# Optimization experiments

Measured on AMD Instinct MI355X. Metric: run time of the kernel, lower is better.

Reference implementation:

```python
import jax, jax.numpy as jnp
import numpy as np

N = 100000
E = 1600000


def _gcn_conv(x, src, dst, norm, W, b, n_nodes):
    # PyG GCNConv: h = x @ W; aggregate normalized messages; add bias.
    h = x @ W                                   # [N, C_out]
    msg = h[src] * norm[:, None]                # [E', C_out] gathered messages
    out = jax.ops.segment_sum(msg, dst, num_segments=n_nodes)
    return out + b


def _norm_coeffs(src, dst, n_nodes):
    # symmetric normalization with self-loops: D^{-1/2} (A+I) D^{-1/2}
    ones = jnp.ones(src.shape[0], dtype=jnp.float32)
    deg = jax.ops.segment_sum(ones, dst, num_segments=n_nodes)
    dis = jnp.where(deg > 0, jax.lax.rsqrt(jnp.maximum(deg, 1.0)), 0.0)
    return dis[src] * dis[dst]


def setup_inputs() -> dict:
    key = jax.random.key(0)
    k1, k2, k3, k4 = jax.random.split(key, 4)
    x = jax.random.normal(k1, (N, 128), dtype=jnp.float32)
    edge_index = jax.random.randint(k2, (2, E), 0, N, dtype=jnp.int64)
    W1 = jax.random.normal(k3, (128, 128), dtype=jnp.float32) * (1.0 / np.sqrt(128))
    b1 = jnp.zeros((128,), dtype=jnp.float32)
    W2 = jax.random.normal(k4, (128, 64), dtype=jnp.float32) * (1.0 / np.sqrt(128))
    b2 = jnp.zeros((64,), dtype=jnp.float32)
    return {"x": x, "edge_index": edge_index, "W1": W1, "b1": b1, "W2": W2, "b2": b2}


def reference(x, edge_index, W1, b1, W2, b2):
    n_nodes = x.shape[0]
    loop = jnp.arange(n_nodes, dtype=edge_index.dtype)
    src = jnp.concatenate([edge_index[0], loop])   # add self-loops
    dst = jnp.concatenate([edge_index[1], loop])
    norm = _norm_coeffs(src, dst, n_nodes)
    h = _gcn_conv(x, src, dst, norm, W1, b1, n_nodes)
    h = jax.nn.relu(h)
    # dropout(p=0.2) is identity in eval mode
    out = _gcn_conv(h, src, dst, norm, W2, b2, n_nodes)
    return out
```

## Files before the change

kernel.cpp:

```cpp
#include <hip/hip_runtime.h>
#include <hip/hip_bf16.h>


typedef short short8v __attribute__((ext_vector_type(8)));
typedef float f32x4   __attribute__((ext_vector_type(4)));

#define BSHIFT 9
#define BSIZE  512
#define CAPSH  14
#define CAP    (1 << CAPSH)

__device__ __forceinline__ short f2bf(float f) {
    unsigned u = __float_as_uint(f);
    return (short)((u + 0x7fffu + ((u >> 16) & 1u)) >> 16);
}
__device__ __forceinline__ unsigned pack2bf(float a, float b) {
    return (unsigned)(unsigned short)f2bf(a) | ((unsigned)(unsigned short)f2bf(b) << 16);
}
__device__ __forceinline__ float bflo(unsigned u) { return __uint_as_float(u << 16); }
__device__ __forceinline__ float bfhi(unsigned u) { return __uint_as_float(u & 0xffff0000u); }

__global__ void k_prep(const float* __restrict__ W1, const float* __restrict__ W2,
                       short* __restrict__ w1t, short* __restrict__ w2t,
                       int* __restrict__ bcur, int nbuck) {
    int b = blockIdx.x;
    int t = threadIdx.x;
    if (b == gridDim.x - 1) {
        if (t < nbuck) bcur[t] = t << CAPSH;
        return;
    }
    int i = b * 256 + t;
    if (i < 128 * 128) {
        int n = i >> 7, k = i & 127;
        w1t[i] = f2bf(W1[k * 128 + n]);
    } else {
        int j = i - 128 * 128;
        int n = j >> 7, k = j & 127;
        w2t[j] = f2bf(W2[k * 64 + n]);
    }
}

__global__ __launch_bounds__(256) void k_bucket(const int* __restrict__ src,
                                                const int* __restrict__ dst,
                                                int* __restrict__ bcur,
                                                unsigned* __restrict__ ebuf,
                                                int E, int nbuck) {
    __shared__ int sdst[4096];
    __shared__ int ssrc[4096];
    __shared__ int hist[256];
    __shared__ int base[256];
    int t = threadIdx.x;
    int e0 = blockIdx.x * 4096;
    for (int i = t; i < nbuck; i += 256) hist[i] = 0;
    for (int i = 0; i < 16; ++i) {
        int k = i * 256 + t;
        int e = e0 + k;
        sdst[k] = (e < E) ? dst[e] : -1;
        ssrc[k] = (e < E) ? src[e] : 0;
    }
    __syncthreads();
    for (int i = 0; i < 16; ++i) {
        int d = sdst[i * 256 + t];
        if (d >= 0) atomicAdd(&hist[d >> BSHIFT], 1);
    }
    __syncthreads();
    for (int b = t; b < nbuck; b += 256) {
        int c = hist[b];
        base[b] = c ? atomicAdd(&bcur[b], c) : 0;
        hist[b] = 0;
    }
    __syncthreads();
    for (int i = 0; i < 16; ++i) {
        int k = i * 256 + t;
        int d = sdst[k];
        if (d >= 0) {
            int bk = d >> BSHIFT;
            int off = atomicAdd(&hist[bk], 1);
            ebuf[base[bk] + off] = ((unsigned)ssrc[k] << BSHIFT) | (unsigned)(d & (BSIZE - 1));
        }
    }
}

__global__ __launch_bounds__(BSIZE) void k_bcsr(const unsigned* __restrict__ ebuf,
                                                const int* __restrict__ bcur,
                                                int* __restrict__ deg,
                                                int* __restrict__ row_ptr,
                                                float* __restrict__ dinv,
                                                unsigned* __restrict__ csr4, int n) {
    __shared__ unsigned edges[CAP];
    __shared__ int hist[BSIZE];
    __shared__ int s[BSIZE];
    __shared__ int cur[BSIZE];
    int b = blockIdx.x;
    int t = threadIdx.x;
    hist[t] = 0;
    __syncthreads();
    int base = b << CAPSH;
    int cnt  = bcur[b] - base;
    int lo = b << BSHIFT;
    for (int k = t; k < cnt; k += BSIZE) {
        unsigned e = ebuf[base + k];
        edges[k] = e;
        atomicAdd(&hist[e & (BSIZE - 1)], 1);
    }
    __syncthreads();
    int v = hist[t];
    s[t] = v;
    __syncthreads();
    for (int off = 1; off < BSIZE; off <<= 1) {
        int add = (t >= off) ? s[t - off] : 0;
        __syncthreads();
        s[t] += add;
        __syncthreads();
    }
    int rp = base + s[t] - v;
    cur[t] = rp;
    int node = lo + t;
    if (node < n) {
        deg[node]     = v;
        row_ptr[node] = rp;
        dinv[node]    = rsqrtf((float)(v + 1));
    }
    __syncthreads();
    for (int k = t; k < cnt; k += BSIZE) {
        unsigned e = edges[k];
        int pos = atomicAdd(&cur[e & (BSIZE - 1)], 1);
        csr4[pos] = e >> BSHIFT;
    }
}

#define LDP 136
__global__ __launch_bounds__(256) void k_gemm1(const float* __restrict__ x,
                                               const short* __restrict__ w1t,
                                               const float* __restrict__ dinv,
                                               short* __restrict__ h, int nrows) {
    __shared__ short xs[64 * LDP];
    __shared__ short wt[128 * LDP];
    int t = threadIdx.x;
    int row0 = blockIdx.x * 64;
    for (int i = 0; i < 16; ++i) {
        int idx = t + i * 256;
        int r = idx >> 5, c4 = idx & 31;
        float4 v = make_float4(0.f, 0.f, 0.f, 0.f);
        if (row0 + r < nrows) v = ((const float4*)x)[(size_t)(row0 + r) * 32 + c4];
        short4 o = make_short4(f2bf(v.x), f2bf(v.y), f2bf(v.z), f2bf(v.w));
        *(short4*)&xs[r * LDP + c4 * 4] = o;
    }
    for (int i = 0; i < 16; ++i) {
        int idx = t + i * 256;
        int n = idx >> 5, c4 = idx & 31;
        *(short4*)&wt[n * LDP + c4 * 4] = ((const short4*)w1t)[idx];
    }
    __syncthreads();
    int wave = t >> 6, lane = t & 63;
    int quad = lane >> 4, c = lane & 15;
    int m0 = wave * 16;
    f32x4 acc[8] = {};
    #pragma unroll
    for (int kc = 0; kc < 4; ++kc) {
        short8v a = *(const short8v*)&xs[(m0 + c) * LDP + kc * 32 + quad * 8];
        #pragma unroll
        for (int nt = 0; nt < 8; ++nt) {
            short8v b = *(const short8v*)&wt[(nt * 16 + c) * LDP + kc * 32 + quad * 8];
            acc[nt] = __builtin_amdgcn_mfma_f32_16x16x32_bf16(a, b, acc[nt], 0, 0, 0);
        }
    }
    #pragma unroll
    for (int r = 0; r < 4; ++r) {
        int row = row0 + m0 + quad * 4 + r;
        if (row < nrows) {
            float dr = dinv[row];
            #pragma unroll
            for (int nt = 0; nt < 8; ++nt)
                h[(size_t)row * 128 + nt * 16 + c] = f2bf(acc[nt][r] * dr);
        }
    }
}

__global__ __launch_bounds__(256) void k_gemm2(const unsigned* __restrict__ aggb,
                                               const float* __restrict__ b1,
                                               const short* __restrict__ w2t,
                                               const float* __restrict__ dinv,
                                               short* __restrict__ h2, int nrows) {
    __shared__ short xs[64 * LDP];
    __shared__ short wt[64 * LDP];
    int t = threadIdx.x;
    int row0 = blockIdx.x * 64;
    for (int i = 0; i < 16; ++i) {
        int idx = t + i * 256;
        int r = idx >> 6, cp = idx & 63;
        unsigned o = 0;
        if (row0 + r < nrows) {
            unsigned u = aggb[(size_t)(row0 + r) * 64 + cp];
            float2 bb = ((const float2*)b1)[cp];
            float vx = fmaxf(bflo(u) + bb.x, 0.f);
            float vy = fmaxf(bfhi(u) + bb.y, 0.f);
            o = pack2bf(vx, vy);
        }
        *(unsigned*)&xs[r * LDP + cp * 2] = o;
    }
    for (int i = 0; i < 8; ++i) {
        int idx = t + i * 256;
        int n = idx >> 5, c4 = idx & 31;
        *(short4*)&wt[n * LDP + c4 * 4] = ((const short4*)w2t)[idx];
    }
    __syncthreads();
    int wave = t >> 6, lane = t & 63;
    int quad = lane >> 4, c = lane & 15;
    int m0 = wave * 16;
    f32x4 acc[4] = {};
    #pragma unroll
    for (int kc = 0; kc < 4; ++kc) {
        short8v av = *(const short8v*)&xs[(m0 + c) * LDP + kc * 32 + quad * 8];
        #pragma unroll
        for (int nt = 0; nt < 4; ++nt) {
            short8v b = *(const short8v*)&wt[(nt * 16 + c) * LDP + kc * 32 + quad * 8];
            acc[nt] = __builtin_amdgcn_mfma_f32_16x16x32_bf16(av, b, acc[nt], 0, 0, 0);
        }
    }
    #pragma unroll
    for (int r = 0; r < 4; ++r) {
        int row = row0 + m0 + quad * 4 + r;
        if (row < nrows) {
            float dr = dinv[row];
            #pragma unroll
            for (int nt = 0; nt < 4; ++nt)
                h2[(size_t)row * 64 + nt * 16 + c] = f2bf(acc[nt][r] * dr);
        }
    }
}

__global__ __launch_bounds__(256) void k_pull128(const unsigned short* __restrict__ h,
                                                 const int* __restrict__ row_ptr,
                                                 const int* __restrict__ deg,
                                                 const unsigned* __restrict__ csr4,
                                                 const float* __restrict__ dinv,
                                                 unsigned* __restrict__ aggb, int n) {
    int wave = (blockIdx.x * 256 + threadIdx.x) >> 6;
    int lane = threadIdx.x & 63;
    if (wave >= n) return;
    int i = __builtin_amdgcn_readfirstlane(wave);
    float2 acc;
    {
        unsigned u = ((const unsigned*)(h + (size_t)i * 128))[lane];
        acc.x = bflo(u);
        acc.y = bfhi(u);
    }
    int beg = row_ptr[i];
    int cnt = deg[i];
    int k = 0;
    for (; k + 8 <= cnt; k += 8) {
        unsigned sid[8];
        unsigned g[8];
        #pragma unroll
        for (int j = 0; j < 8; ++j) sid[j] = csr4[beg + k + j];
        #pragma unroll
        for (int j = 0; j < 8; ++j)
            g[j] = ((const unsigned*)(h + (size_t)sid[j] * 128))[lane];
        #pragma unroll
        for (int j = 0; j < 8; ++j) {
            acc.x += bflo(g[j]);
            acc.y += bfhi(g[j]);
        }
    }
    for (; k < cnt; ++k) {
        unsigned sid = csr4[beg + k];
        unsigned g = ((const unsigned*)(h + (size_t)sid * 128))[lane];
        acc.x += bflo(g);
        acc.y += bfhi(g);
    }
    float di = dinv[i];
    aggb[(size_t)i * 64 + lane] = pack2bf(acc.x * di, acc.y * di);
}

__global__ __launch_bounds__(256) void k_pull64(const unsigned short* __restrict__ h,
                                                const int* __restrict__ row_ptr,
                                                const int* __restrict__ deg,
                                                const unsigned* __restrict__ csr4,
                                                const float* __restrict__ dinv,
                                                const float* __restrict__ b2,
                                                float* __restrict__ out, int n) {
    int wave = (blockIdx.x * 256 + threadIdx.x) >> 6;
    int lane = threadIdx.x & 63;
    if (wave >= n) return;
    int i = __builtin_amdgcn_readfirstlane(wave);
    float acc = __uint_as_float((unsigned)h[(size_t)i * 64 + lane] << 16);
    int beg = row_ptr[i];
    int cnt = deg[i];
    int k = 0;
    for (; k + 8 <= cnt; k += 8) {
        unsigned sid[8];
        unsigned short u[8];
        #pragma unroll
        for (int j = 0; j < 8; ++j) sid[j] = csr4[beg + k + j];
        #pragma unroll
        for (int j = 0; j < 8; ++j) u[j] = h[(size_t)sid[j] * 64 + lane];
        #pragma unroll
        for (int j = 0; j < 8; ++j)
            acc += __uint_as_float((unsigned)u[j] << 16);
    }
    for (; k < cnt; ++k) {
        unsigned sid = csr4[beg + k];
        acc += __uint_as_float((unsigned)h[(size_t)sid * 64 + lane] << 16);
    }
    out[(size_t)i * 64 + lane] = acc * dinv[i] + b2[lane];
}

extern "C" void kernel_launch(void* const* d_in, const int* in_sizes, int n_in,
                              void* d_out, int out_size, void* d_ws, size_t ws_size,
                              hipStream_t stream) {
    const float* x  = (const float*)d_in[0];
    const int*   ei = (const int*)d_in[1];
    const float* W1 = (const float*)d_in[2];
    const float* b1 = (const float*)d_in[3];
    const float* W2 = (const float*)d_in[4];
    const float* b2 = (const float*)d_in[5];
    float* out = (float*)d_out;

    const int N = in_sizes[0] / 128;
    const int E = in_sizes[1] / 2;
    const int* src = ei;
    const int* dst = ei + E;
    const int nbuck = (N + BSIZE - 1) >> BSHIFT;
    const size_t capE = (size_t)nbuck << CAPSH;

    float* dinv     = (float*)d_ws;
    int*   deg      = (int*)(dinv + N);
    int*   row_ptr  = deg + N;
    int*   bcur     = row_ptr + N;
    short* w1t      = (short*)(bcur + 256);
    short* w2t      = w1t + 128 * 128;
    unsigned* csr4  = (unsigned*)(w2t + 64 * 128);
    short* bufH     = (short*)(csr4 + capE);
    short* bufH2    = bufH + (size_t)N * 128;
    unsigned* aggb  = (unsigned*)(bufH2 + (size_t)N * 64);
    unsigned* ebuf  = (unsigned*)bufH2;

    const int ntile = (E + 4095) / 4096;

    k_prep<<<97, 256, 0, stream>>>(W1, W2, w1t, w2t, bcur, nbuck);

    k_bucket<<<ntile, 256, 0, stream>>>(src, dst, bcur, ebuf, E, nbuck);
    k_bcsr<<<nbuck, BSIZE, 0, stream>>>(ebuf, bcur, deg, row_ptr, dinv, csr4, N);

    k_gemm1<<<(N + 63) / 64, 256, 0, stream>>>(x, w1t, dinv, bufH, N);
    k_pull128<<<(N + 3) / 4, 256, 0, stream>>>((const unsigned short*)bufH, row_ptr, deg, csr4, dinv, aggb, N);

    k_gemm2<<<(N + 63) / 64, 256, 0, stream>>>(aggb, b1, w2t, dinv, bufH2, N);
    k_pull64<<<(N + 3) / 4, 256, 0, stream>>>((const unsigned short*)bufH2, row_ptr, deg, csr4, dinv, b2, out, N);
}
```

Baseline: 291.7 us.

## Split layer-1 features into column-chunk slabs for cache-local gather

The layer-1 hidden features and aggregation buffer are stored as 8 column slabs of 16 bf16 (32 bytes) per node instead of row-major 256-byte rows. The pull kernel now assigns 8 lanes per node and launches 8 chunk-blocks per node group, so each block gathers only from one slab (a 3.2MB working set) to improve L2/MALL hit rates. Neighbor indices are loaded once per group and broadcast with shuffles, and nontemporal loads and stores are used. Each gather is now a small 32-byte segment and the index list is re-read 8 times, which risks more memory transactions.

```diff
diff --git a/kernel.cpp b/kernel.cpp
--- a/kernel.cpp
+++ b/kernel.cpp
@@ -165,6 +165,7 @@
             acc[nt] = __builtin_amdgcn_mfma_f32_16x16x32_bf16(a, b, acc[nt], 0, 0, 0);
         }
     }
+    size_t slab = (size_t)nrows * 16;
     #pragma unroll
     for (int r = 0; r < 4; ++r) {
         int row = row0 + m0 + quad * 4 + r;
@@ -172,7 +173,7 @@
             float dr = dinv[row];
             #pragma unroll
             for (int nt = 0; nt < 8; ++nt)
-                h[(size_t)row * 128 + nt * 16 + c] = f2bf(acc[nt][r] * dr);
+                h[(size_t)nt * slab + (size_t)row * 16 + c] = f2bf(acc[nt][r] * dr);
         }
     }
 }
@@ -186,12 +187,13 @@
     __shared__ short wt[64 * LDP];
     int t = threadIdx.x;
     int row0 = blockIdx.x * 64;
+    size_t slab8 = (size_t)nrows * 8;
     for (int i = 0; i < 16; ++i) {
         int idx = t + i * 256;
         int r = idx >> 6, cp = idx & 63;
         unsigned o = 0;
         if (row0 + r < nrows) {
-            unsigned u = aggb[(size_t)(row0 + r) * 64 + cp];
+            unsigned u = aggb[(size_t)(cp >> 3) * slab8 + (size_t)(row0 + r) * 8 + (cp & 7)];
             float2 bb = ((const float2*)b1)[cp];
             float vx = fmaxf(bflo(u) + bb.x, 0.f);
             float vy = fmaxf(bfhi(u) + bb.y, 0.f);
@@ -230,33 +232,41 @@
     }
 }
 
-__global__ __launch_bounds__(256) void k_pull128(const unsigned short* __restrict__ h,
+__global__ __launch_bounds__(256) void k_pull128(const unsigned* __restrict__ h,
                                                  const int* __restrict__ row_ptr,
                                                  const int* __restrict__ deg,
                                                  const unsigned* __restrict__ csr4,
                                                  const float* __restrict__ dinv,
-                                                 unsigned* __restrict__ aggb, int n) {
-    int wave = (blockIdx.x * 256 + threadIdx.x) >> 6;
-    int lane = threadIdx.x & 63;
-    if (wave >= n) return;
-    int i = __builtin_amdgcn_readfirstlane(wave);
+                                                 unsigned* __restrict__ aggb,
+                                                 int n) {
+    int chunk = blockIdx.x & 7;
+    int nb    = blockIdx.x >> 3;
+    int t = threadIdx.x;
+    int lane = t & 63;
+    int wv   = t >> 6;
+    int grp  = lane >> 3;
+    int sub  = lane & 7;
+    int i = nb * 32 + wv * 8 + grp;
+    if (i >= n) return;
+    const unsigned* hc = h + (size_t)chunk * n * 8;
     float2 acc;
     {
-        unsigned u = ((const unsigned*)(h + (size_t)i * 128))[lane];
+        unsigned u = hc[(size_t)i * 8 + sub];
         acc.x = bflo(u);
         acc.y = bfhi(u);
     }
-    int beg = row_ptr[i];
-    int cnt = deg[i];
+    int beg = __builtin_nontemporal_load(&row_ptr[i]);
+    int cnt = __builtin_nontemporal_load(&deg[i]);
+    int base = lane & ~7;
     int k = 0;
     for (; k + 8 <= cnt; k += 8) {
-        unsigned sid[8];
+        int sidv = (int)__builtin_nontemporal_load(&csr4[beg + k + sub]);
         unsigned g[8];
         #pragma unroll
-        for (int j = 0; j < 8; ++j) sid[j] = csr4[beg + k + j];
-        #pragma unroll
-        for (int j = 0; j < 8; ++j)
-            g[j] = ((const unsigned*)(h + (size_t)sid[j] * 128))[lane];
+        for (int j = 0; j < 8; ++j) {
+            unsigned s = (unsigned)__shfl(sidv, base + j);
+            g[j] = hc[(size_t)s * 8 + sub];
+        }
         #pragma unroll
         for (int j = 0; j < 8; ++j) {
             acc.x += bflo(g[j]);
@@ -264,13 +274,14 @@
         }
     }
     for (; k < cnt; ++k) {
-        unsigned sid = csr4[beg + k];
-        unsigned g = ((const unsigned*)(h + (size_t)sid * 128))[lane];
+        unsigned s = csr4[beg + k];
+        unsigned g = hc[(size_t)s * 8 + sub];
         acc.x += bflo(g);
         acc.y += bfhi(g);
     }
-    float di = dinv[i];
-    aggb[(size_t)i * 64 + lane] = pack2bf(acc.x * di, acc.y * di);
+    float di = __builtin_nontemporal_load(&dinv[i]);
+    unsigned* ab = aggb + (size_t)chunk * n * 8;
+    __builtin_nontemporal_store(pack2bf(acc.x * di, acc.y * di), &ab[(size_t)i * 8 + sub]);
 }
 
 __global__ __launch_bounds__(256) void k_pull64(const unsigned short* __restrict__ h,
@@ -344,7 +355,7 @@
     k_bcsr<<<nbuck, BSIZE, 0, stream>>>(ebuf, bcur, deg, row_ptr, dinv, csr4, N);
 
     k_gemm1<<<(N + 63) / 64, 256, 0, stream>>>(x, w1t, dinv, bufH, N);
-    k_pull128<<<(N + 3) / 4, 256, 0, stream>>>((const unsigned short*)bufH, row_ptr, deg, csr4, dinv, aggb, N);
+    k_pull128<<<8 * ((N + 31) / 32), 256, 0, stream>>>((const unsigned*)bufH, row_ptr, deg, csr4, dinv, aggb, N);
 
     k_gemm2<<<(N + 63) / 64, 256, 0, stream>>>(aggb, b1, w2t, dinv, bufH2, N);
     k_pull64<<<(N + 3) / 4, 256, 0, stream>>>((const unsigned short*)bufH2, row_ptr, deg, csr4, dinv, b2, out, N);
```

Result: slower. 367.7 us (+26.1%).
